# Kernel optimization log

Hardware: AMD Instinct MI355X
Metric: run time of the kernel (lower is better)

## Reference

```python
import jax, jax.numpy as jnp
import numpy as np

B, E, R, HSZ, HEADS, PROP, RTOKS = 16, 400, 624, 512, 4, 2, 40
N = E + R            # nodes per graph = entities + relations
DFF = HSZ * HEADS    # Block FFN width (l1: hsz -> hsz*heads)


def setup_inputs() -> dict:
    key = jax.random.key(0)
    ks = jax.random.split(key, 12)
    ents = jax.random.normal(ks[0], (B, E, HSZ), jnp.float32)
    rels = jax.random.randint(ks[1], (B, R), 0, RTOKS)
    adj = jax.random.randint(ks[2], (B, N, N), 0, 2)
    # self-loops so no softmax row is fully masked
    d = jnp.arange(N)
    adj = adj.at[:, d, d].set(1)
    renc = jax.random.normal(ks[3], (RTOKS, HSZ)) * (2.0 / (RTOKS + HSZ)) ** 0.5

    def lin(k, fi, fo):  # weights stored (in, out): y = x @ W + b
        return jax.random.normal(k, (PROP, fi, fo)) * (1.0 / fi) ** 0.5

    Wq = lin(ks[4], HSZ, HSZ)
    Wk = lin(ks[5], HSZ, HSZ)
    Wv = lin(ks[6], HSZ, HSZ)
    l1_w = lin(ks[7], HSZ, DFF)
    l1_b = jnp.zeros((PROP, DFF))
    l2_w = lin(ks[8], DFF, HSZ)
    l2_b = jnp.zeros((PROP, HSZ))
    ln1_s = jnp.ones((PROP, HSZ)); ln1_b = jnp.zeros((PROP, HSZ))
    ln2_s = jnp.ones((PROP, HSZ)); ln2_b = jnp.zeros((PROP, HSZ))
    prelu_a = jnp.full((PROP, DFF), 0.25)
    return dict(ents=ents, rels=rels, adj=adj, renc=renc, Wq=Wq, Wk=Wk, Wv=Wv,
                l1_w=l1_w, l1_b=l1_b, l2_w=l2_w, l2_b=l2_b,
                ln1_s=ln1_s, ln1_b=ln1_b, ln2_s=ln2_s, ln2_b=ln2_b,
                prelu_a=prelu_a)


def _layer_norm(x, s, b, eps=1e-5):
    mu = jnp.mean(x, -1, keepdims=True)
    var = jnp.mean((x - mu) ** 2, -1, keepdims=True)
    return (x - mu) * jax.lax.rsqrt(var + eps) * s + b


def _mha(q, kv, adj, Wq, Wk, Wv):
    # GraphWriter MultiHeadAttention: split heads by contiguous chunks,
    # scale by sqrt(key_dim)=sqrt(HSZ), mask where adj==0, residual += query.
    dk = HSZ // HEADS
    Q = (q @ Wq).reshape(B, N, HEADS, dk)
    K = (kv @ Wk).reshape(B, N, HEADS, dk)
    V = (kv @ Wv).reshape(B, N, HEADS, dk)
    scores = jnp.einsum('bnhd,bmhd->bhnm', Q, K) / np.sqrt(HSZ).astype(np.float32)
    scores = jnp.where((adj == 0)[:, None, :, :], -jnp.inf, scores)
    attn = jax.nn.softmax(scores, axis=-1)
    out = jnp.einsum('bhnm,bmhd->bnhd', attn, V).reshape(B, N, HSZ)
    return out + q


def _encode(ents, rels, adj, renc, Wq, Wk, Wv, l1_w, l1_b, l2_w, l2_b,
            ln1_s, ln1_b, ln2_s, ln2_b, prelu_a):
    x = jnp.concatenate([ents, renc[rels]], axis=1)  # (B, N, HSZ)
    for j in range(PROP):  # fixed small number of propagation Blocks
        kv = jax.lax.stop_gradient(x)  # dense path wraps kv in torch.tensor(requires_grad=False)
        out = _mha(x, kv, adj, Wq[j], Wk[j], Wv[j])
        t = _layer_norm(out, ln1_s[j], ln1_b[j])
        h = t @ l1_w[j] + l1_b[j]
        h = jnp.maximum(h, 0) + prelu_a[j] * jnp.minimum(h, 0)  # PReLU
        h = h @ l2_w[j] + l2_b[j]  # dropout p=0 (eval)
        x = _layer_norm(h + t, ln2_s[j], ln2_b[j])
    return x


def reference(ents, rels, adj, renc, Wq, Wk, Wv, l1_w, l1_b, l2_w, l2_b,
              ln1_s, ln1_b, ln2_s, ln2_b, prelu_a):
    nodes = _encode(ents, rels, adj, renc, Wq, Wk, Wv, l1_w, l1_b, l2_w, l2_b,
                    ln1_s, ln1_b, ln2_s, ln2_b, prelu_a)
    glob = nodes[:, E]  # node at index ent_lens[i] (first relation node)
    node_mask = jnp.ones((B, N), dtype=bool)  # ent_lens uniform -> all valid
    return glob, nodes, node_mask
```

## Files before the change

### kernel.cpp

```cpp
#include <hip/hip_runtime.h>
#include <hip/hip_bf16.h>

typedef __bf16 bf16;
typedef __attribute__((ext_vector_type(8))) bf16 bf16x8;
typedef __attribute__((ext_vector_type(4))) float f32x4;

constexpr int B_   = 16;
constexpr int E_   = 400;
constexpr int R_   = 624;
constexpr int N_   = 1024;
constexpr int HSZ_ = 512;
constexpr int DFF_ = 2048;
constexpr int M_   = B_ * N_;

__device__ __forceinline__ void glds16(const void* g, void* l) {
    __builtin_amdgcn_global_load_lds((const __attribute__((address_space(1))) void*)g,
                                     (__attribute__((address_space(3))) void*)l,
                                     16, 0, 0);
}

__global__ __launch_bounds__(256) void transpose_f32_bf16(const float* __restrict__ in,
                                                          bf16* __restrict__ out,
                                                          int rows, int cols) {
    __shared__ float tile[32][33];
    int c0 = blockIdx.x * 32, r0 = blockIdx.y * 32;
    int tx = threadIdx.x, ty = threadIdx.y;
    #pragma unroll
    for (int i = 0; i < 32; i += 8)
        tile[ty + i][tx] = in[(size_t)(r0 + ty + i) * cols + (c0 + tx)];
    __syncthreads();
    #pragma unroll
    for (int i = 0; i < 32; i += 8)
        out[(size_t)(c0 + ty + i) * rows + (r0 + tx)] = (bf16)tile[tx][ty + i];
}

__global__ __launch_bounds__(256) void pack_adj(const int* __restrict__ adj,
                                                unsigned* __restrict__ adjw) {
    int gid  = blockIdx.x * 4 + (threadIdx.x >> 6);
    int lane = threadIdx.x & 63;
    int w64  = gid & 15;
    int bn   = gid >> 4;
    int v = adj[(size_t)bn * N_ + w64 * 64 + lane];
    unsigned long long mask = __ballot(v != 0);
    if (lane == 0)  adjw[bn * 32 + w64 * 2]     = (unsigned)mask;
    if (lane == 32) adjw[bn * 32 + w64 * 2 + 1] = (unsigned)(mask >> 32);
}

__global__ __launch_bounds__(256) void build_x(const float* __restrict__ ents,
                                               const int* __restrict__ rels,
                                               const float* __restrict__ renc,
                                               bf16* __restrict__ x) {
    int idx  = blockIdx.x * 256 + threadIdx.x;
    int col8 = (idx & 63) * 8;
    int row  = idx >> 6;
    int b = row >> 10, n = row & 1023;
    const float* src;
    if (n < E_) src = ents + ((size_t)(b * E_ + n)) * HSZ_ + col8;
    else {
        int rt = rels[b * R_ + (n - E_)];
        src = renc + (size_t)rt * HSZ_ + col8;
    }
    float4 a = *(const float4*)src;
    float4 c = *(const float4*)(src + 4);
    bf16x8 v;
    v[0] = (bf16)a.x; v[1] = (bf16)a.y; v[2] = (bf16)a.z; v[3] = (bf16)a.w;
    v[4] = (bf16)c.x; v[5] = (bf16)c.y; v[6] = (bf16)c.z; v[7] = (bf16)c.w;
    *(bf16x8*)(x + (size_t)row * HSZ_ + col8) = v;
}

template <int MODE>
__global__ __launch_bounds__(256) void gemm_bt(const bf16* __restrict__ A,
                                               const bf16* __restrict__ Bt,
                                               const float* __restrict__ biasF,
                                               const float* __restrict__ alphaF,
                                               const bf16* __restrict__ extraB,
                                               bf16* __restrict__ outB,
                                               bf16* __restrict__ outB2,
                                               bf16* __restrict__ outB3,
                                               float* __restrict__ outF,
                                               int Nn, int Kk) {
    __shared__ bf16 As[128][64];
    __shared__ bf16 Bs[128][64];

    int nwg = gridDim.x * gridDim.y;
    int bid = blockIdx.y * gridDim.x + blockIdx.x;
    int q = nwg >> 3;
    int ng = (bid & 7) * q + (bid >> 3);
    int bx = ng % gridDim.x, by = ng / gridDim.x;

    int n0 = bx * 128, m0 = by * 128;
    int t = threadIdx.x;
    int lane = t & 63, r = lane & 15, quad = lane >> 4;
    int w = t >> 6;
    int wm = w >> 1, wn = w & 1;

    int sRow = t >> 3;
    int xr   = sRow & 7;
    int sColL = (t & 7) * 8;
    int sColG = ((t & 7) ^ xr) * 8;
    const bf16* Ag = A  + (size_t)(m0 + sRow) * Kk + sColG;
    const bf16* Bg = Bt + (size_t)(n0 + sRow) * Kk + sColG;

#define G_STAGE(k0_) do {                                          \
        glds16(Ag + (k0_),           &As[sRow     ][sColL]);       \
        glds16(Ag + 32 * Kk + (k0_), &As[sRow + 32][sColL]);       \
        glds16(Ag + 64 * Kk + (k0_), &As[sRow + 64][sColL]);       \
        glds16(Ag + 96 * Kk + (k0_), &As[sRow + 96][sColL]);       \
        glds16(Bg + (k0_),           &Bs[sRow     ][sColL]);       \
        glds16(Bg + 32 * Kk + (k0_), &Bs[sRow + 32][sColL]);       \
        glds16(Bg + 64 * Kk + (k0_), &Bs[sRow + 64][sColL]);       \
        glds16(Bg + 96 * Kk + (k0_), &Bs[sRow + 96][sColL]);       \
    } while (0)

    f32x4 acc[4][4];
    #pragma unroll
    for (int mt = 0; mt < 4; mt++)
        #pragma unroll
        for (int nt = 0; nt < 4; nt++) acc[mt][nt] = (f32x4){0.f, 0.f, 0.f, 0.f};

    int xa = r & 7;

    for (int k0 = 0; k0 < Kk; k0 += 64) {
        G_STAGE(k0);
        __syncthreads();
        #pragma unroll
        for (int kk = 0; kk < 64; kk += 32) {
            int pc = (((kk >> 3) + quad) ^ xa) * 8;
            bf16x8 af[4], bfr[4];
            #pragma unroll
            for (int mt = 0; mt < 4; mt++)
                af[mt] = *(const bf16x8*)&As[wm * 64 + mt * 16 + r][pc];
            #pragma unroll
            for (int nt = 0; nt < 4; nt++)
                bfr[nt] = *(const bf16x8*)&Bs[wn * 64 + nt * 16 + r][pc];
            #pragma unroll
            for (int mt = 0; mt < 4; mt++)
                #pragma unroll
                for (int nt = 0; nt < 4; nt++)
                    acc[mt][nt] = __builtin_amdgcn_mfma_f32_16x16x32_bf16(af[mt], bfr[nt], acc[mt][nt], 0, 0, 0);
        }
        __syncthreads();
    }
#undef G_STAGE

    #pragma unroll
    for (int mt = 0; mt < 4; mt++) {
        #pragma unroll
        for (int nt = 0; nt < 4; nt++) {
            #pragma unroll
            for (int i = 0; i < 4; i++) {
                int rg = m0 + wm * 64 + mt * 16 + quad * 4 + i;
                int cg = n0 + wn * 64 + nt * 16 + r;
                float v = acc[mt][nt][i];
                if (MODE == 0) {
                    outB[(size_t)rg * Nn + cg] = (bf16)v;
                } else if (MODE == 1) {
                    int bb = rg >> 10, n = rg & 1023;
                    outB[(size_t)(bb * HSZ_ + cg) * N_ + n] = (bf16)v;
                } else if (MODE == 2) {
                    v += biasF[cg];
                    float a = alphaF[cg];
                    v = v > 0.f ? v : a * v;
                    outB[(size_t)rg * Nn + cg] = (bf16)v;
                } else if (MODE == 3) {
                    v += biasF[cg] + (float)extraB[(size_t)rg * Nn + cg];
                    outF[(size_t)rg * Nn + cg] = v;
                } else {
                    if (cg < 512) {
                        outB[(size_t)rg * HSZ_ + cg] = (bf16)v;
                    } else if (cg < 1024) {
                        outB2[(size_t)rg * HSZ_ + (cg - 512)] = (bf16)v;
                    } else {
                        int bb = rg >> 10, n = rg & 1023;
                        outB3[(size_t)(bb * HSZ_ + (cg - 1024)) * N_ + n] = (bf16)v;
                    }
                }
            }
        }
    }
}

__global__ __launch_bounds__(256) void attn_fused(const bf16* __restrict__ Q,
                                                  const bf16* __restrict__ K,
                                                  const bf16* __restrict__ Vt,
                                                  const unsigned* __restrict__ adjw,
                                                  const bf16* __restrict__ xb,
                                                  float* __restrict__ tpre) {
    int blk = blockIdx.x;
    int gr = blk & 7;
    int qb = (blk >> 3) & 7;
    int gq = blk >> 6;
    int g = gq * 8 + gr;
    int b = g >> 2, h = g & 3;

    int tid = threadIdx.x;
    int w = tid >> 6, lane = tid & 63;
    int r = lane & 15, quad = lane >> 4;
    int n0 = qb * 128 + w * 32;

    __shared__ bf16 Ks[64][136];
    __shared__ bf16 Vs[128][72];
    __shared__ bf16 plds[4][32][68];

    int kRow = tid >> 4, kCol = (tid & 15) * 8;
    int vRow = tid >> 3, vCol = (tid & 7) * 8;
    const bf16* Kg = K + (size_t)(b * N_) * HSZ_ + h * 128 + (size_t)kRow * HSZ_ + kCol;
    const bf16* Vg = Vt + (size_t)(b * HSZ_ + h * 128 + vRow) * N_ + vCol;
    bf16* KsP = &Ks[kRow][kCol];
    bf16* VsP = &Vs[vRow][vCol];

    uint4 kp0, kp1, kp2, kp3, vp0, vp1, vp2, vp3;

#define ATTN_ISSUE(it_) do {                                                      \
        const bf16* kg_ = Kg + (size_t)(it_) * 64 * HSZ_;                         \
        const bf16* vg_ = Vg + (it_) * 64;                                        \
        kp0 = *(const uint4*)(kg_);                                               \
        kp1 = *(const uint4*)(kg_ + 16 * HSZ_);                                   \
        kp2 = *(const uint4*)(kg_ + 32 * HSZ_);                                   \
        kp3 = *(const uint4*)(kg_ + 48 * HSZ_);                                   \
        vp0 = *(const uint4*)(vg_);                                               \
        vp1 = *(const uint4*)(vg_ + 32 * N_);                                     \
        vp2 = *(const uint4*)(vg_ + 64 * N_);                                     \
        vp3 = *(const uint4*)(vg_ + 96 * N_);                                     \
    } while (0)

#define ATTN_COMMIT() do {                                                        \
        *(uint4*)(KsP)            = kp0;                                          \
        *(uint4*)(KsP + 16 * 136) = kp1;                                          \
        *(uint4*)(KsP + 32 * 136) = kp2;                                          \
        *(uint4*)(KsP + 48 * 136) = kp3;                                          \
        *(uint4*)(VsP)            = vp0;                                          \
        *(uint4*)(VsP + 32 * 72)  = vp1;                                          \
        *(uint4*)(VsP + 64 * 72)  = vp2;                                          \
        *(uint4*)(VsP + 96 * 72)  = vp3;                                          \
    } while (0)

    bf16x8 qf[2][4];
    #pragma unroll
    for (int mt = 0; mt < 2; mt++) {
        const bf16* qbase = Q + ((size_t)(b * N_ + n0 + mt * 16 + r)) * HSZ_ + h * 128;
        #pragma unroll
        for (int kc = 0; kc < 4; kc++) qf[mt][kc] = *(const bf16x8*)(qbase + kc * 32 + quad * 8);
    }

    f32x4 accv[2][8];
    #pragma unroll
    for (int mt = 0; mt < 2; mt++)
        #pragma unroll
        for (int dt = 0; dt < 8; dt++) accv[mt][dt] = (f32x4){0.f, 0.f, 0.f, 0.f};
    float tl[2][4] = {{0.f, 0.f, 0.f, 0.f}, {0.f, 0.f, 0.f, 0.f}};
    const float scale = 0.04419417382415922f;
    const float SHIFT = 12.0f;

    ATTN_ISSUE(0);
    for (int it = 0; it < 16; it++) {
        __syncthreads();
        ATTN_COMMIT();
        __syncthreads();
        if (it + 1 < 16) ATTN_ISSUE(it + 1);

        f32x4 cg[2][4];
        #pragma unroll
        for (int mt = 0; mt < 2; mt++)
            #pragma unroll
            for (int gk = 0; gk < 4; gk++) cg[mt][gk] = (f32x4){0.f, 0.f, 0.f, 0.f};
        __builtin_amdgcn_s_setprio(1);
        #pragma unroll
        for (int gk = 0; gk < 4; gk++)
            #pragma unroll
            for (int kc = 0; kc < 4; kc++) {
                bf16x8 kf = *(const bf16x8*)&Ks[gk * 16 + r][kc * 32 + quad * 8];
                cg[0][gk] = __builtin_amdgcn_mfma_f32_16x16x32_bf16(qf[0][kc], kf, cg[0][gk], 0, 0, 0);
                cg[1][gk] = __builtin_amdgcn_mfma_f32_16x16x32_bf16(qf[1][kc], kf, cg[1][gk], 0, 0, 0);
            }
        __builtin_amdgcn_s_setprio(0);
        #pragma unroll
        for (int mt = 0; mt < 2; mt++)
            #pragma unroll
            for (int i = 0; i < 4; i++) {
                int row_l = mt * 16 + quad * 4 + i;
                int row_g = n0 + row_l;
                const unsigned* aw = &adjw[((size_t)(b << 10) + row_g) * 32 + it * 2];
                unsigned wb0 = aw[0], wb1 = aw[1];
                float p0 = ((wb0 >> r) & 1u)        ? __expf(cg[mt][0][i] * scale - SHIFT) : 0.f;
                float p1 = ((wb0 >> (16 + r)) & 1u) ? __expf(cg[mt][1][i] * scale - SHIFT) : 0.f;
                float p2 = ((wb1 >> r) & 1u)        ? __expf(cg[mt][2][i] * scale - SHIFT) : 0.f;
                float p3 = ((wb1 >> (16 + r)) & 1u) ? __expf(cg[mt][3][i] * scale - SHIFT) : 0.f;
                tl[mt][i] += p0 + p1 + p2 + p3;
                plds[w][row_l][r]      = (bf16)p0;
                plds[w][row_l][16 + r] = (bf16)p1;
                plds[w][row_l][32 + r] = (bf16)p2;
                plds[w][row_l][48 + r] = (bf16)p3;
            }

        bf16x8 pf00 = *(const bf16x8*)&plds[w][r][quad * 8];
        bf16x8 pf01 = *(const bf16x8*)&plds[w][r][32 + quad * 8];
        bf16x8 pf10 = *(const bf16x8*)&plds[w][16 + r][quad * 8];
        bf16x8 pf11 = *(const bf16x8*)&plds[w][16 + r][32 + quad * 8];
        __builtin_amdgcn_s_setprio(1);
        #pragma unroll
        for (int dt = 0; dt < 8; dt++) {
            bf16x8 v0 = *(const bf16x8*)&Vs[dt * 16 + r][quad * 8];
            bf16x8 v1 = *(const bf16x8*)&Vs[dt * 16 + r][32 + quad * 8];
            accv[0][dt] = __builtin_amdgcn_mfma_f32_16x16x32_bf16(pf00, v0, accv[0][dt], 0, 0, 0);
            accv[0][dt] = __builtin_amdgcn_mfma_f32_16x16x32_bf16(pf01, v1, accv[0][dt], 0, 0, 0);
            accv[1][dt] = __builtin_amdgcn_mfma_f32_16x16x32_bf16(pf10, v0, accv[1][dt], 0, 0, 0);
            accv[1][dt] = __builtin_amdgcn_mfma_f32_16x16x32_bf16(pf11, v1, accv[1][dt], 0, 0, 0);
        }
        __builtin_amdgcn_s_setprio(0);
    }
#undef ATTN_ISSUE
#undef ATTN_COMMIT

    #pragma unroll
    for (int mt = 0; mt < 2; mt++)
        #pragma unroll
        for (int i = 0; i < 4; i++) {
            float l = tl[mt][i];
            #pragma unroll
            for (int d = 1; d < 16; d <<= 1) l += __shfl_xor(l, d, 64);
            float inv_l = 1.0f / fmaxf(l, 1e-30f);
            #pragma unroll
            for (int dt = 0; dt < 8; dt++) {
                int row = n0 + mt * 16 + quad * 4 + i;
                int col = h * 128 + dt * 16 + r;
                size_t idx = ((size_t)(b * N_ + row)) * HSZ_ + col;
                tpre[idx] = accv[mt][dt][i] * inv_l + (float)xb[idx];
            }
        }
}

__global__ __launch_bounds__(256) void lnorm_k(const float* __restrict__ in,
                                               const float* __restrict__ sc,
                                               const float* __restrict__ bi,
                                               bf16* __restrict__ out) {
    int row = blockIdx.x * 4 + (threadIdx.x >> 6);
    int lane = threadIdx.x & 63;
    const float* rp = in + (size_t)row * HSZ_;
    float4 a = *(const float4*)(rp + lane * 4);
    float4 b = *(const float4*)(rp + 256 + lane * 4);
    float sum = a.x + a.y + a.z + a.w + b.x + b.y + b.z + b.w;
    float sq  = a.x*a.x + a.y*a.y + a.z*a.z + a.w*a.w
              + b.x*b.x + b.y*b.y + b.z*b.z + b.w*b.w;
    #pragma unroll
    for (int d = 1; d < 64; d <<= 1) {
        sum += __shfl_xor(sum, d, 64);
        sq  += __shfl_xor(sq,  d, 64);
    }
    float mu = sum * (1.0f / HSZ_);
    float varv = fmaxf(sq * (1.0f / HSZ_) - mu * mu, 0.f);
    float rs = rsqrtf(varv + 1e-5f);
    bf16* op = out + (size_t)row * HSZ_;
    int c0 = lane * 4;
    float va[4] = {a.x, a.y, a.z, a.w}, vb[4] = {b.x, b.y, b.z, b.w};
    #pragma unroll
    for (int k = 0; k < 4; k++) {
        op[c0 + k]       = (bf16)(((va[k] - mu) * rs) * sc[c0 + k] + bi[c0 + k]);
        op[c0 + 256 + k] = (bf16)(((vb[k] - mu) * rs) * sc[c0 + 256 + k] + bi[c0 + 256 + k]);
    }
}

__global__ __launch_bounds__(256) void write_out(const bf16* __restrict__ x,
                                                 float* __restrict__ out) {
    size_t tid = (size_t)blockIdx.x * 256 + threadIdx.x;
    if (tid < (size_t)B_ * HSZ_) {
        int b = (int)(tid >> 9), c = (int)(tid & 511);
        out[tid] = (float)x[((size_t)(b * N_ + E_)) * HSZ_ + c];
    } else if (tid < (size_t)B_ * HSZ_ + (size_t)B_ * N_ * HSZ_) {
        out[tid] = (float)x[tid - B_ * HSZ_];
    } else {
        out[tid] = 1.0f;
    }
}

extern "C" void kernel_launch(void* const* d_in, const int* in_sizes, int n_in,
                              void* d_out, int out_size, void* d_ws, size_t ws_size,
                              hipStream_t stream) {
    const float* ents = (const float*)d_in[0];
    const int*   rels = (const int*)d_in[1];
    const int*   adj  = (const int*)d_in[2];
    const float* renc = (const float*)d_in[3];
    const float* Wq   = (const float*)d_in[4];
    const float* Wk   = (const float*)d_in[5];
    const float* Wv   = (const float*)d_in[6];
    const float* l1w  = (const float*)d_in[7];
    const float* l1b  = (const float*)d_in[8];
    const float* l2w  = (const float*)d_in[9];
    const float* l2b  = (const float*)d_in[10];
    const float* ln1s = (const float*)d_in[11];
    const float* ln1b = (const float*)d_in[12];
    const float* ln2s = (const float*)d_in[13];
    const float* ln2b = (const float*)d_in[14];
    const float* pa   = (const float*)d_in[15];

    char* ws = (char*)d_ws;
    size_t o = 0;
    auto alloc = [&](size_t bytes) { void* p = ws + o; o += bytes; return p; };
    bf16*     WqkvT  = (bf16*)alloc(3145728);
    bf16*     L1T    = (bf16*)alloc(4194304);
    bf16*     L2T    = (bf16*)alloc(4194304);
    unsigned* adjw   = (unsigned*)alloc(2097152);
    bf16*     xb     = (bf16*)alloc(16777216);
    bf16*     Qb     = (bf16*)alloc(16777216);
    bf16*     Kb     = (bf16*)alloc(16777216);
    bf16*     Vt     = (bf16*)alloc(16777216);
    bf16*     tb     = (bf16*)alloc(16777216);
    bf16*     hb     = (bf16*)alloc(67108864);
    float*    f32buf = (float*)alloc(33554432);
    if (o > ws_size) return;

    dim3 t32(32, 8);
    for (int j = 0; j < 2; j++) {
        transpose_f32_bf16<<<dim3(16, 16), t32, 0, stream>>>(Wq  + j * 262144,  WqkvT + j * 786432,          512, 512);
        transpose_f32_bf16<<<dim3(16, 16), t32, 0, stream>>>(Wk  + j * 262144,  WqkvT + j * 786432 + 262144, 512, 512);
        transpose_f32_bf16<<<dim3(16, 16), t32, 0, stream>>>(Wv  + j * 262144,  WqkvT + j * 786432 + 524288, 512, 512);
        transpose_f32_bf16<<<dim3(64, 16), t32, 0, stream>>>(l1w + j * 1048576, L1T + j * 1048576, 512, 2048);
        transpose_f32_bf16<<<dim3(16, 64), t32, 0, stream>>>(l2w + j * 1048576, L2T + j * 1048576, 2048, 512);
    }
    pack_adj<<<65536, 256, 0, stream>>>(adj, adjw);
    build_x<<<4096, 256, 0, stream>>>(ents, rels, renc, xb);

    for (int j = 0; j < 2; j++) {
        gemm_bt<4><<<dim3(12, 128), 256, 0, stream>>>(xb, WqkvT + j * 786432, nullptr, nullptr, nullptr,
                                                      Qb, Kb, Vt, nullptr, 1536, 512);
        attn_fused<<<512, 256, 0, stream>>>(Qb, Kb, Vt, adjw, xb, f32buf);
        lnorm_k<<<4096, 256, 0, stream>>>(f32buf, ln1s + j * 512, ln1b + j * 512, tb);
        gemm_bt<2><<<dim3(16, 128), 256, 0, stream>>>(tb, L1T + j * 1048576, l1b + j * 2048, pa + j * 2048,
                                                      nullptr, hb, nullptr, nullptr, nullptr, 2048, 512);
        gemm_bt<3><<<dim3(4, 128), 256, 0, stream>>>(hb, L2T + j * 1048576, l2b + j * 512, nullptr,
                                                     tb, nullptr, nullptr, nullptr, f32buf, 512, 2048);
        lnorm_k<<<4096, 256, 0, stream>>>(f32buf, ln2s + j * 512, ln2b + j * 512, xb);
    }
    write_out<<<32864, 256, 0, stream>>>(xb, (float*)d_out);
}
```

Baseline: 698.1 us.

## Double-buffer LDS tiles in gemm_bt to overlap global loads with MFMA

The GEMM kernel now keeps two LDS buffers for the A and B tiles. It issues the global-to-LDS loads for the next K tile before computing on the current one, with an explicit vmcnt wait that leaves the 8 newest loads in flight. This hides global memory latency behind MFMA work. In exchange, LDS use doubles to 64KB per block, which may lower occupancy, and correctness now depends on the manual waitcnt and barrier placement.

Result: faster. 670.1 us (-4.0%).

```diff
diff --git a/kernel.cpp b/kernel.cpp
--- a/kernel.cpp
+++ b/kernel.cpp
@@ -79,8 +79,8 @@
                                                bf16* __restrict__ outB3,
                                                float* __restrict__ outF,
                                                int Nn, int Kk) {
-    __shared__ bf16 As[128][64];
-    __shared__ bf16 Bs[128][64];
+    __shared__ bf16 As[2][128][64];
+    __shared__ bf16 Bs[2][128][64];
 
     int nwg = gridDim.x * gridDim.y;
     int bid = blockIdx.y * gridDim.x + blockIdx.x;
@@ -101,15 +101,15 @@
     const bf16* Ag = A  + (size_t)(m0 + sRow) * Kk + sColG;
     const bf16* Bg = Bt + (size_t)(n0 + sRow) * Kk + sColG;
 
-#define G_STAGE(k0_) do {                                          \
-        glds16(Ag + (k0_),           &As[sRow     ][sColL]);       \
-        glds16(Ag + 32 * Kk + (k0_), &As[sRow + 32][sColL]);       \
-        glds16(Ag + 64 * Kk + (k0_), &As[sRow + 64][sColL]);       \
-        glds16(Ag + 96 * Kk + (k0_), &As[sRow + 96][sColL]);       \
-        glds16(Bg + (k0_),           &Bs[sRow     ][sColL]);       \
-        glds16(Bg + 32 * Kk + (k0_), &Bs[sRow + 32][sColL]);       \
-        glds16(Bg + 64 * Kk + (k0_), &Bs[sRow + 64][sColL]);       \
-        glds16(Bg + 96 * Kk + (k0_), &Bs[sRow + 96][sColL]);       \
+#define G_STAGE(p_, k0_) do {                                          \
+        glds16(Ag + (k0_),           &As[p_][sRow     ][sColL]);       \
+        glds16(Ag + 32 * Kk + (k0_), &As[p_][sRow + 32][sColL]);       \
+        glds16(Ag + 64 * Kk + (k0_), &As[p_][sRow + 64][sColL]);       \
+        glds16(Ag + 96 * Kk + (k0_), &As[p_][sRow + 96][sColL]);       \
+        glds16(Bg + (k0_),           &Bs[p_][sRow     ][sColL]);       \
+        glds16(Bg + 32 * Kk + (k0_), &Bs[p_][sRow + 32][sColL]);       \
+        glds16(Bg + 64 * Kk + (k0_), &Bs[p_][sRow + 64][sColL]);       \
+        glds16(Bg + 96 * Kk + (k0_), &Bs[p_][sRow + 96][sColL]);       \
     } while (0)
 
     f32x4 acc[4][4];
@@ -120,26 +120,36 @@
 
     int xa = r & 7;
 
-    for (int k0 = 0; k0 < Kk; k0 += 64) {
-        G_STAGE(k0);
-        __syncthreads();
+    G_STAGE(0, 0);
+    int ntiles = Kk >> 6;
+    for (int tt = 0; tt < ntiles; tt++) {
+        int p = tt & 1;
+        if (tt + 1 < ntiles) {
+            G_STAGE(p ^ 1, (tt + 1) * 64);
+            asm volatile("s_waitcnt vmcnt(8)" ::: "memory");
+        } else {
+            asm volatile("s_waitcnt vmcnt(0)" ::: "memory");
+        }
+        __builtin_amdgcn_s_barrier();
+        __builtin_amdgcn_sched_barrier(0);
         #pragma unroll
         for (int kk = 0; kk < 64; kk += 32) {
             int pc = (((kk >> 3) + quad) ^ xa) * 8;
             bf16x8 af[4], bfr[4];
             #pragma unroll
             for (int mt = 0; mt < 4; mt++)
-                af[mt] = *(const bf16x8*)&As[wm * 64 + mt * 16 + r][pc];
+                af[mt] = *(const bf16x8*)&As[p][wm * 64 + mt * 16 + r][pc];
             #pragma unroll
             for (int nt = 0; nt < 4; nt++)
-                bfr[nt] = *(const bf16x8*)&Bs[wn * 64 + nt * 16 + r][pc];
+                bfr[nt] = *(const bf16x8*)&Bs[p][wn * 64 + nt * 16 + r][pc];
             #pragma unroll
             for (int mt = 0; mt < 4; mt++)
                 #pragma unroll
                 for (int nt = 0; nt < 4; nt++)
                     acc[mt][nt] = __builtin_amdgcn_mfma_f32_16x16x32_bf16(af[mt], bfr[nt], acc[mt][nt], 0, 0, 0);
         }
-        __syncthreads();
+        __builtin_amdgcn_s_barrier();
+        __builtin_amdgcn_sched_barrier(0);
     }
 #undef G_STAGE
 
```
